# Optimization experiments

Hardware: AMD Instinct MI355X
Metric: run time of the kernel (lower is better)

## Reference

```python
import jax, jax.numpy as jnp
import numpy as np

N_HEAD = 16
N_EMBD = 2048
HEAD_DIM = N_EMBD // N_HEAD


def setup_inputs() -> dict:
    key = jax.random.key(0)
    kx, kqkv, kp = jax.random.split(key, 3)
    B, S = 2, 2048
    x = jax.random.normal(kx, (B, S, N_EMBD), dtype=jnp.float32)
    # torch nn.Linear weights, stored as [out, in]; y = x @ W.T
    scale = 1.0 / np.sqrt(N_EMBD)
    Wqkv = jax.random.uniform(kqkv, (3 * N_EMBD, N_EMBD), dtype=jnp.float32, minval=-scale, maxval=scale)
    Wproj = jax.random.uniform(kp, (N_EMBD, N_EMBD), dtype=jnp.float32, minval=-scale, maxval=scale)
    return {"x": x, "Wqkv": Wqkv, "Wproj": Wproj}


def reference(x, Wqkv, Wproj):
    B, S, E = x.shape
    qkv = x @ Wqkv.T  # [B,S,3E]
    q, k, v = jnp.split(qkv, 3, axis=2)
    # [B,H,S,D]
    q = q.reshape(B, S, N_HEAD, HEAD_DIM).transpose(0, 2, 1, 3)
    k = k.reshape(B, S, N_HEAD, HEAD_DIM).transpose(0, 2, 1, 3)
    v = v.reshape(B, S, N_HEAD, HEAD_DIM).transpose(0, 2, 1, 3)
    scores = jnp.einsum('bhqd,bhkd->bhqk', q, k) / jnp.sqrt(jnp.float32(HEAD_DIM))
    causal = jnp.tril(jnp.ones((S, S), dtype=bool))  # [S,S]
    scores = jnp.where(causal[None, None, :, :], scores, -jnp.inf)
    weights = jax.nn.softmax(scores, axis=-1)
    out = jnp.einsum('bhqk,bhkd->bhqd', weights, v)  # [B,H,S,D]
    out = out.transpose(0, 2, 1, 3).reshape(B, S, E)
    return out @ Wproj.T
```

## Files before the change

kernel.cpp:

```cpp
#include <hip/hip_runtime.h>
#include <cstdint>
#include <cstddef>

typedef __bf16 bf16;
typedef __bf16 bf16x8 __attribute__((ext_vector_type(8)));
typedef float  f32x4  __attribute__((ext_vector_type(4)));

static_assert(sizeof(bf16x8) == 16, "bf16x8 must be 16B");

__device__ __forceinline__ void async_copy16(const bf16* g, bf16* l) {
  __builtin_amdgcn_global_load_lds(
      (__attribute__((address_space(1))) void*)(g),
      (__attribute__((address_space(3))) void*)(l),
      16, 0, 0);
}

__device__ __forceinline__ uint32_t lds_u32(const bf16* p) {
  return (uint32_t)(uintptr_t)((__attribute__((address_space(3))) const bf16*)p);
}

__global__ __launch_bounds__(256)
void conv_f32_bf16(const float* __restrict__ s, bf16* __restrict__ d) {
  const size_t i = ((size_t)blockIdx.x * 256 + threadIdx.x) * 8;
  const f32x4 a = *(const f32x4*)(s + i);
  const f32x4 b = *(const f32x4*)(s + i + 4);
  bf16x8 o;
#pragma unroll
  for (int e = 0; e < 4; ++e) { o[e] = (bf16)a[e]; o[4 + e] = (bf16)b[e]; }
  *(bf16x8*)(d + i) = o;
}

template<int AMODE>
__device__ __forceinline__ void stageA32(const bf16* __restrict__ P, int K,
                                         int row0, int k0,
                                         bf16* lds, int wave, int lane) {
  const int lin0 = wave * 64;
  const int lin  = lin0 + lane;
  const int row  = lin >> 2;
  const int ch   = lin & 3;
  const int gch  = ch ^ ((row >> 1) & 3);
  const bf16* src;
  if constexpr (AMODE == 2) {
    const int rowA = row0 + row;
    const int b = rowA >> 11, s = rowA & 2047;
    src = P + ((size_t)(b * 16 + (k0 >> 7)) * 2048 + s) * 128 + (k0 & 127) + gch * 8;
  } else {
    src = P + (size_t)(row0 + row) * K + k0 + gch * 8;
  }
  async_copy16(src, lds + lin0 * 8);
}

__device__ __forceinline__ void stageW32(const bf16* __restrict__ P, int K,
                                         int row0, int k0,
                                         bf16* lds, int wave, int lane) {
#pragma unroll
  for (int i = 0; i < 2; ++i) {
    const int lin0 = i * 512 + wave * 64;
    const int lin  = lin0 + lane;
    const int row  = lin >> 2;
    const int ch   = lin & 3;
    const int gch  = ch ^ ((row >> 1) & 3);
    async_copy16(P + (size_t)(row0 + row) * K + k0 + gch * 8,
                 lds + lin0 * 8);
  }
}

__device__ __forceinline__ void ld_frags(uint32_t ab, uint32_t bb,
                                         bf16x8 (&a)[4], bf16x8 (&b)[4]) {
  asm volatile("ds_read_b128 %0, %1 offset:0"    : "=v"(a[0]) : "v"(ab));
  asm volatile("ds_read_b128 %0, %1 offset:1024" : "=v"(a[1]) : "v"(ab));
  asm volatile("ds_read_b128 %0, %1 offset:2048" : "=v"(a[2]) : "v"(ab));
  asm volatile("ds_read_b128 %0, %1 offset:3072" : "=v"(a[3]) : "v"(ab));
  asm volatile("ds_read_b128 %0, %1 offset:0"    : "=v"(b[0]) : "v"(bb));
  asm volatile("ds_read_b128 %0, %1 offset:1024" : "=v"(b[1]) : "v"(bb));
  asm volatile("ds_read_b128 %0, %1 offset:2048" : "=v"(b[2]) : "v"(bb));
  asm volatile("ds_read_b128 %0, %1 offset:3072" : "=v"(b[3]) : "v"(bb));
}

template<int AMODE, int CMODE>
__global__ __launch_bounds__(512, 2)
void gemm_bt3(const bf16* __restrict__ A, const bf16* __restrict__ W,
              float* __restrict__ Crow, bf16* __restrict__ Cq,
              bf16* __restrict__ Ck, bf16* __restrict__ Cvt,
              int M, int N, int K, int nbase) {
  __shared__ bf16 As[5][128 * 32];
  __shared__ bf16 Ws[5][256 * 32];

  const int tid  = threadIdx.x;
  const int wave = tid >> 6, lane = tid & 63;
  const int quad = lane >> 4, r = lane & 15;
  const int wr = wave >> 2, wc = wave & 3;

  const int gx  = gridDim.x;
  const int nwg = gx * gridDim.y;
  int wg = blockIdx.y * gx + blockIdx.x;
  wg = (wg & 7) * (nwg >> 3) + (wg >> 3);
  const int m0 = (wg / gx) * 128;
  const int n0 = (wg % gx) * 256;

  const int wm = wr * 64, wn = wc * 64;
  const int nT = K >> 5;
  const int cs = quad ^ ((r >> 1) & 3);

  f32x4 acc[4][4] = {};

  const uint32_t a_rd = lds_u32(&As[0][0]) + (((wm + r) * 32 + cs * 8) << 1);
  const uint32_t b_rd = lds_u32(&Ws[0][0]) + (((wn + r) * 32 + cs * 8) << 1);

#pragma unroll
  for (int i = 0; i < 4; ++i)
    if (i < nT) {
      stageA32<AMODE>(A, K, m0, i << 5, &As[i][0], wave, lane);
      stageW32(W, K, n0, i << 5, &Ws[i][0], wave, lane);
    }
  if (nT > 3)       asm volatile("s_waitcnt vmcnt(9)" ::: "memory");
  else if (nT == 3) asm volatile("s_waitcnt vmcnt(6)" ::: "memory");
  else if (nT == 2) asm volatile("s_waitcnt vmcnt(3)" ::: "memory");
  else              asm volatile("s_waitcnt vmcnt(0)" ::: "memory");
  __builtin_amdgcn_sched_barrier(0);
  __builtin_amdgcn_s_barrier();

  int bc = 0;
  int bs = 4;
  for (int t = 0; t < nT; ++t) {
    bf16x8 af[4], bw[4];
    ld_frags(a_rd + bc * 8192, b_rd + bc * 16384, af, bw);
    if (t + 4 < nT) {
      stageA32<AMODE>(A, K, m0, (t + 4) << 5, &As[bs][0], wave, lane);
      stageW32(W, K, n0, (t + 4) << 5, &Ws[bs][0], wave, lane);
      asm volatile("s_waitcnt vmcnt(9)" ::: "memory");
    } else if (t + 4 == nT) {
      asm volatile("s_waitcnt vmcnt(6)" ::: "memory");
    } else if (t + 3 == nT) {
      asm volatile("s_waitcnt vmcnt(3)" ::: "memory");
    } else {
      asm volatile("s_waitcnt vmcnt(0)" ::: "memory");
    }
    __builtin_amdgcn_sched_barrier(0);
    asm volatile("s_waitcnt lgkmcnt(0)" ::: "memory");
    __builtin_amdgcn_sched_barrier(0);
    __builtin_amdgcn_s_setprio(1);
#pragma unroll
    for (int m = 0; m < 4; ++m)
#pragma unroll
      for (int n = 0; n < 4; ++n)
        acc[m][n] = __builtin_amdgcn_mfma_f32_16x16x32_bf16(af[m], bw[n], acc[m][n], 0, 0, 0);
    __builtin_amdgcn_s_setprio(0);
    __builtin_amdgcn_s_barrier();
    bc = (bc + 1 == 5) ? 0 : bc + 1;
    bs = (bs + 1 == 5) ? 0 : bs + 1;
  }

#pragma unroll
  for (int i = 0; i < 4; ++i) {
    const int growb = m0 + wm + i * 16 + quad * 4;
#pragma unroll
    for (int j = 0; j < 4; ++j) {
      const int gcol = n0 + wn + j * 16 + r;
#pragma unroll
      for (int rg = 0; rg < 4; ++rg) {
        const int grow = growb + rg;
        if constexpr (CMODE == 1) {
          const int gc = nbase + gcol;
          const int which = gc >> 11;
          const int h = (gc >> 7) & 15;
          const int d = gc & 127;
          const int b = grow >> 11;
          const int s = grow & 2047;
          const bf16 v = (bf16)acc[i][j][rg];
          if (which == 0)
            Cq[(((size_t)b * 16 + h) * 2048 + s) * 128 + d] = v;
          else if (which == 1)
            Ck[(((size_t)b * 16 + h) * 2048 + s) * 128 + d] = v;
          else
            Cvt[(((size_t)b * 16 + h) * 128 + d) * 2048 + s] = v;
        } else {
          Crow[(size_t)grow * N + gcol] = acc[i][j][rg];
        }
      }
    }
  }
}

__global__ __launch_bounds__(256, 2)
void attn_kernel(bf16* __restrict__ Q, const bf16* __restrict__ K,
                 const bf16* __restrict__ Vt, int S) {
  __shared__ bf16 k_lds[2][64 * 128];
  __shared__ bf16 v_lds[2][128 * 64];
  __shared__ bf16 p_lds[4][16 * 64];

  const int tid = threadIdx.x, wave = tid >> 6, lane = tid & 63;
  const int quad = lane >> 4, r = lane & 15;
  const int bh = blockIdx.y;
  bf16* Qh = Q + (size_t)bh * S * 128;
  const bf16* Kh = K + (size_t)bh * S * 128;
  const bf16* Vth = Vt + (size_t)bh * 128 * S;

  const float sc = 0.0883883476483184f * 1.4426950408889634f;

  auto issue_stage = [&](int kv0, int buf) {
#pragma unroll
    for (int j = 0; j < 4; ++j) {
      const int lin0 = j * 256 + wave * 64;
      const int lin = lin0 + lane;
      const int row = lin >> 4, ch = lin & 15;
      async_copy16(Kh + (size_t)(kv0 + row) * 128 + ((ch ^ (row & 7)) << 3),
                   &k_lds[buf][0] + lin0 * 8);
    }
#pragma unroll
    for (int j = 0; j < 4; ++j) {
      const int lin0 = j * 256 + wave * 64;
      const int lin = lin0 + lane;
      const int row = lin >> 3, c = lin & 7;
      async_copy16(Vth + (size_t)row * S + kv0 + ((c ^ (row & 7)) << 3),
                   &v_lds[buf][0] + lin0 * 8);
    }
  };

  for (int pass = 0; pass < 2; ++pass) {
    const int qb = pass ? blockIdx.x : (31 - blockIdx.x);
    const int q0 = qb << 6;
    const int qrow0 = q0 + wave * 16;
    const int nkv = qb + 1;

    bf16x8 qf[4];
    for (int ks = 0; ks < 4; ++ks)
      qf[ks] = *(const bf16x8*)(Qh + (size_t)(qrow0 + r) * 128 + ks * 32 + quad * 8);

    f32x4 o_acc[8] = {};
    f32x4 m_run, l_run;
    for (int t = 0; t < 4; ++t) { m_run[t] = -1e30f; l_run[t] = 0.f; }

    issue_stage(0, 0);

    for (int kt = 0; kt < nkv; ++kt) {
      const int kv0 = kt << 6;
      const int cur = kt & 1;
      if (kt + 1 < nkv) {
        issue_stage((kt + 1) << 6, cur ^ 1);
        asm volatile("s_waitcnt vmcnt(8)" ::: "memory");
      } else {
        asm volatile("s_waitcnt vmcnt(0)" ::: "memory");
      }
      __builtin_amdgcn_sched_barrier(0);
      __syncthreads();

      {
        f32x4 sa[4] = {};
        __builtin_amdgcn_s_setprio(1);
        for (int ks = 0; ks < 4; ++ks) {
          bf16x8 kf[4];
          for (int nt = 0; nt < 4; ++nt) {
            const int kr = nt * 16 + r;
            kf[nt] = *(const bf16x8*)(&k_lds[cur][0] + kr * 128 + (((ks * 4 + quad) ^ (kr & 7)) << 3));
          }
          for (int nt = 0; nt < 4; ++nt)
            sa[nt] = __builtin_amdgcn_mfma_f32_16x16x32_bf16(qf[ks], kf[nt], sa[nt], 0, 0, 0);
        }
        __builtin_amdgcn_s_setprio(0);
        if (kv0 + 63 > qrow0) {
          for (int nt = 0; nt < 4; ++nt) {
            const int col  = kv0 + nt * 16 + r;
            const int rowb = qrow0 + quad * 4;
            for (int rg = 0; rg < 4; ++rg)
              if (col > rowb + rg) sa[nt][rg] = -1e30f;
          }
        }
        f32x4 mx = sa[0];
        for (int nt = 1; nt < 4; ++nt)
          for (int rg = 0; rg < 4; ++rg) mx[rg] = fmaxf(mx[rg], sa[nt][rg]);
        for (int off = 1; off < 16; off <<= 1)
          for (int rg = 0; rg < 4; ++rg) mx[rg] = fmaxf(mx[rg], __shfl_xor(mx[rg], off, 64));
        float need = mx[0] - m_run[0];
        for (int rg = 1; rg < 4; ++rg) need = fmaxf(need, mx[rg] - m_run[rg]);
        if (need * sc > 8.0f) {
          f32x4 alpha;
          for (int rg = 0; rg < 4; ++rg) {
            const float mnew = fmaxf(m_run[rg], mx[rg]);
            alpha[rg] = exp2f((m_run[rg] - mnew) * sc);
            m_run[rg] = mnew;
            l_run[rg] *= alpha[rg];
          }
          for (int nt2 = 0; nt2 < 8; ++nt2)
            for (int rg = 0; rg < 4; ++rg) o_acc[nt2][rg] *= alpha[rg];
        }
        f32x4 rsum = {0.f, 0.f, 0.f, 0.f};
        for (int nt = 0; nt < 4; ++nt)
          for (int rg = 0; rg < 4; ++rg) {
            const float p = exp2f((sa[nt][rg] - m_run[rg]) * sc);
            sa[nt][rg] = p;
            rsum[rg] += p;
          }
        for (int off = 1; off < 16; off <<= 1)
          for (int rg = 0; rg < 4; ++rg) rsum[rg] += __shfl_xor(rsum[rg], off, 64);
        for (int rg = 0; rg < 4; ++rg) l_run[rg] += rsum[rg];
        for (int nt = 0; nt < 4; ++nt)
          for (int rg = 0; rg < 4; ++rg) {
            const int prow = quad * 4 + rg;
            const int pcol = nt * 16 + r;
            p_lds[wave][prow * 64 + (((pcol >> 3) ^ (prow & 7)) * 8) + (pcol & 7)] =
                (bf16)sa[nt][rg];
          }
        __builtin_amdgcn_s_setprio(1);
        for (int ks2 = 0; ks2 < 2; ++ks2) {
          const int prow = r;
          const bf16x8 pf = *(const bf16x8*)(p_lds[wave] + prow * 64 + (((ks2 * 4 + quad) ^ (prow & 7)) * 8));
          for (int nt2 = 0; nt2 < 8; ++nt2) {
            const int vrow = nt2 * 16 + r;
            const bf16x8 vf = *(const bf16x8*)(&v_lds[cur][0] + vrow * 64 + (((ks2 * 4 + quad) ^ (vrow & 7)) * 8));
            o_acc[nt2] = __builtin_amdgcn_mfma_f32_16x16x32_bf16(pf, vf, o_acc[nt2], 0, 0, 0);
          }
        }
        __builtin_amdgcn_s_setprio(0);
      }
      __syncthreads();
    }

    f32x4 inv;
    for (int rg = 0; rg < 4; ++rg) inv[rg] = 1.0f / l_run[rg];
    for (int nt2 = 0; nt2 < 8; ++nt2) {
      const int d = nt2 * 16 + r;
      for (int rg = 0; rg < 4; ++rg) {
        const int s = qrow0 + quad * 4 + rg;
        Qh[(size_t)s * 128 + d] = (bf16)(o_acc[nt2][rg] * inv[rg]);
      }
    }
  }
}

extern "C" void kernel_launch(void* const* d_in, const int* in_sizes, int n_in,
                              void* d_out, int out_size, void* d_ws, size_t ws_size,
                              hipStream_t stream) {
  const float* x     = (const float*)d_in[0];
  const float* Wqkv  = (const float*)d_in[1];
  const float* Wproj = (const float*)d_in[2];
  float* out = (float*)d_out;

  const int Bm = 4096, E = 2048;
  const size_t plane = 8388608;

  bf16* qw  = (bf16*)d_ws;
  bf16* vtw = qw + plane;
  bf16* xb  = vtw + plane;
  bf16* kw  = (bf16*)d_out;
  bf16* wqb = kw + plane;

  conv_f32_bf16<<<8388608 / 2048, 256, 0, stream>>>(x, xb);
  for (int chunk = 0; chunk < 3; ++chunk) {
    conv_f32_bf16<<<4194304 / 2048, 256, 0, stream>>>(Wqkv + (size_t)chunk * 4194304, wqb);
    gemm_bt3<0, 1><<<dim3(2048 / 256, Bm / 128), 512, 0, stream>>>(
        xb, wqb, nullptr, qw, kw, vtw, Bm, 2048, E, chunk * 2048);
  }
  attn_kernel<<<dim3(16, 32), 256, 0, stream>>>(qw, kw, vtw, 2048);
  conv_f32_bf16<<<4194304 / 2048, 256, 0, stream>>>(Wproj, xb);
  gemm_bt3<2, 0><<<dim3(2048 / 256, Bm / 128), 512, 0, stream>>>(
      qw, xb, out, nullptr, nullptr, nullptr, Bm, 2048, E, 0);
}
```

Baseline: 401.0 us.

## Add 256x256 four-stage GEMM for output projection and split attention launch

Adds a new GEMM kernel with 256x256 tiles, a four-buffer async LDS pipeline, swizzled layout, workgroup remapping and explicit waitcnt scheduling. It replaces the 256x128 GEMM for the output projection. The attention launch is split into two launches of 8 query-block pairs each, using an added ibase offset. The larger tile increases operand reuse per byte loaded but uses more LDS, which limits occupancy, and the attention split adds a launch.

```diff
diff --git a/kernel.cpp b/kernel.cpp
--- a/kernel.cpp
+++ b/kernel.cpp
@@ -182,9 +182,150 @@
   }
 }
 
+template<int AMODE>
+__device__ __forceinline__ void stage256(const bf16* __restrict__ P, int K,
+                                         int row0, int k0,
+                                         bf16* lds, int wave, int lane) {
+#pragma unroll
+  for (int i = 0; i < 2; ++i) {
+    const int lin0 = i * 512 + wave * 64;
+    const int lin  = lin0 + lane;
+    const int row  = lin >> 2;
+    const int ch   = lin & 3;
+    const int gch  = ch ^ ((row >> 1) & 3);
+    const bf16* src;
+    if constexpr (AMODE == 2) {
+      const int rowA = row0 + row;
+      const int b = rowA >> 11, s = rowA & 2047;
+      src = P + ((size_t)(b * 16 + (k0 >> 7)) * 2048 + s) * 128 + (k0 & 127) + gch * 8;
+    } else {
+      src = P + (size_t)(row0 + row) * K + k0 + gch * 8;
+    }
+    async_copy16(src, lds + lin0 * 8);
+  }
+}
+
+__device__ __forceinline__ void ld_frags84(uint32_t ab, uint32_t bb,
+                                           bf16x8 (&a)[8], bf16x8 (&b)[4]) {
+  asm volatile("ds_read_b128 %0, %1 offset:0"    : "=v"(a[0]) : "v"(ab));
+  asm volatile("ds_read_b128 %0, %1 offset:1024" : "=v"(a[1]) : "v"(ab));
+  asm volatile("ds_read_b128 %0, %1 offset:2048" : "=v"(a[2]) : "v"(ab));
+  asm volatile("ds_read_b128 %0, %1 offset:3072" : "=v"(a[3]) : "v"(ab));
+  asm volatile("ds_read_b128 %0, %1 offset:4096" : "=v"(a[4]) : "v"(ab));
+  asm volatile("ds_read_b128 %0, %1 offset:5120" : "=v"(a[5]) : "v"(ab));
+  asm volatile("ds_read_b128 %0, %1 offset:6144" : "=v"(a[6]) : "v"(ab));
+  asm volatile("ds_read_b128 %0, %1 offset:7168" : "=v"(a[7]) : "v"(ab));
+  asm volatile("ds_read_b128 %0, %1 offset:0"    : "=v"(b[0]) : "v"(bb));
+  asm volatile("ds_read_b128 %0, %1 offset:1024" : "=v"(b[1]) : "v"(bb));
+  asm volatile("ds_read_b128 %0, %1 offset:2048" : "=v"(b[2]) : "v"(bb));
+  asm volatile("ds_read_b128 %0, %1 offset:3072" : "=v"(b[3]) : "v"(bb));
+}
+
+template<int AMODE, int CMODE>
+__global__ __launch_bounds__(512, 2)
+void gemm256r(const bf16* __restrict__ A, const bf16* __restrict__ W,
+              float* __restrict__ Crow, bf16* __restrict__ Cq,
+              bf16* __restrict__ Ck, bf16* __restrict__ Cvt,
+              int M, int N, int K, int nbase) {
+  __shared__ bf16 As[4][256 * 32];
+  __shared__ bf16 Ws[4][256 * 32];
+
+  const int tid  = threadIdx.x;
+  const int wave = tid >> 6, lane = tid & 63;
+  const int quad = lane >> 4, r = lane & 15;
+  const int wr = wave >> 2, wc = wave & 3;
+
+  const int gx  = gridDim.x;
+  const int nwg = gx * gridDim.y;
+  int wg = blockIdx.y * gx + blockIdx.x;
+  wg = (wg & 7) * (nwg >> 3) + (wg >> 3);
+  const int m0 = (wg / gx) * 256;
+  const int n0 = (wg % gx) * 256;
+
+  const int wm = wr * 128, wn = wc * 64;
+  const int nT = K >> 5;
+  const int cs = quad ^ ((r >> 1) & 3);
+
+  f32x4 acc[8][4] = {};
+
+  const uint32_t a_rd = lds_u32(&As[0][0]) + (((wm + r) * 32 + cs * 8) << 1);
+  const uint32_t b_rd = lds_u32(&Ws[0][0]) + (((wn + r) * 32 + cs * 8) << 1);
+
+#pragma unroll
+  for (int i = 0; i < 3; ++i)
+    if (i < nT) {
+      stage256<AMODE>(A, K, m0, i << 5, &As[i][0], wave, lane);
+      stage256<0>(W, K, n0, i << 5, &Ws[i][0], wave, lane);
+    }
+  if (nT > 2)       asm volatile("s_waitcnt vmcnt(8)" ::: "memory");
+  else if (nT == 2) asm volatile("s_waitcnt vmcnt(4)" ::: "memory");
+  else              asm volatile("s_waitcnt vmcnt(0)" ::: "memory");
+  __builtin_amdgcn_sched_barrier(0);
+  __builtin_amdgcn_s_barrier();
+
+  int bc = 0;
+  int bs = 3;
+  for (int t = 0; t < nT; ++t) {
+    bf16x8 af[8], bw[4];
+    ld_frags84(a_rd + bc * 16384, b_rd + bc * 16384, af, bw);
+    if (t + 3 < nT) {
+      stage256<AMODE>(A, K, m0, (t + 3) << 5, &As[bs][0], wave, lane);
+      stage256<0>(W, K, n0, (t + 3) << 5, &Ws[bs][0], wave, lane);
+      asm volatile("s_waitcnt vmcnt(8)" ::: "memory");
+    } else if (t + 3 == nT) {
+      asm volatile("s_waitcnt vmcnt(4)" ::: "memory");
+    } else {
+      asm volatile("s_waitcnt vmcnt(0)" ::: "memory");
+    }
+    __builtin_amdgcn_sched_barrier(0);
+    asm volatile("s_waitcnt lgkmcnt(0)" ::: "memory");
+    __builtin_amdgcn_sched_barrier(0);
+    __builtin_amdgcn_s_setprio(1);
+#pragma unroll
+    for (int m = 0; m < 8; ++m)
+#pragma unroll
+      for (int n = 0; n < 4; ++n)
+        acc[m][n] = __builtin_amdgcn_mfma_f32_16x16x32_bf16(af[m], bw[n], acc[m][n], 0, 0, 0);
+    __builtin_amdgcn_s_setprio(0);
+    __builtin_amdgcn_s_barrier();
+    bc = (bc + 1) & 3;
+    bs = (bs + 1) & 3;
+  }
+
+#pragma unroll
+  for (int i = 0; i < 8; ++i) {
+    const int growb = m0 + wm + i * 16 + quad * 4;
+#pragma unroll
+    for (int j = 0; j < 4; ++j) {
+      const int gcol = n0 + wn + j * 16 + r;
+#pragma unroll
+      for (int rg = 0; rg < 4; ++rg) {
+        const int grow = growb + rg;
+        if constexpr (CMODE == 1) {
+          const int gc = nbase + gcol;
+          const int which = gc >> 11;
+          const int h = (gc >> 7) & 15;
+          const int d = gc & 127;
+          const int b = grow >> 11;
+          const int s = grow & 2047;
+          const bf16 v = (bf16)acc[i][j][rg];
+          if (which == 0)
+            Cq[(((size_t)b * 16 + h) * 2048 + s) * 128 + d] = v;
+          else if (which == 1)
+            Ck[(((size_t)b * 16 + h) * 2048 + s) * 128 + d] = v;
+          else
+            Cvt[(((size_t)b * 16 + h) * 128 + d) * 2048 + s] = v;
+        } else {
+          Crow[(size_t)grow * N + gcol] = acc[i][j][rg];
+        }
+      }
+    }
+  }
+}
+
 __global__ __launch_bounds__(256, 2)
 void attn_kernel(bf16* __restrict__ Q, const bf16* __restrict__ K,
-                 const bf16* __restrict__ Vt, int S) {
+                 const bf16* __restrict__ Vt, int S, int ibase) {
   __shared__ bf16 k_lds[2][64 * 128];
   __shared__ bf16 v_lds[2][128 * 64];
   __shared__ bf16 p_lds[4][16 * 64];
@@ -217,8 +358,9 @@
     }
   };
 
+  const int i0 = ibase + blockIdx.x;
   for (int pass = 0; pass < 2; ++pass) {
-    const int qb = pass ? blockIdx.x : (31 - blockIdx.x);
+    const int qb = pass ? i0 : (31 - i0);
     const int q0 = qb << 6;
     const int qrow0 = q0 + wave * 16;
     const int nkv = qb + 1;
@@ -351,8 +493,9 @@
     gemm_bt3<0, 1><<<dim3(2048 / 256, Bm / 128), 512, 0, stream>>>(
         xb, wqb, nullptr, qw, kw, vtw, Bm, 2048, E, chunk * 2048);
   }
-  attn_kernel<<<dim3(16, 32), 256, 0, stream>>>(qw, kw, vtw, 2048);
+  attn_kernel<<<dim3(8, 32), 256, 0, stream>>>(qw, kw, vtw, 2048, 0);
+  attn_kernel<<<dim3(8, 32), 256, 0, stream>>>(qw, kw, vtw, 2048, 8);
   conv_f32_bf16<<<4194304 / 2048, 256, 0, stream>>>(Wproj, xb);
-  gemm_bt3<2, 0><<<dim3(2048 / 256, Bm / 128), 512, 0, stream>>>(
+  gemm256r<2, 0><<<dim3(2048 / 256, Bm / 256), 512, 0, stream>>>(
       qw, xb, out, nullptr, nullptr, nullptr, Bm, 2048, E, 0);
 }
```

Measured after the change: 478.1 us. 19.2% more time.

## Load K/V fragments directly from global memory and remap blocks for L2 locality

Applied to the files above, without the earlier changes.

Removes the double-buffered LDS staging of K and V tiles, with its async copies, waitcnts and block-wide barriers. Each wave now reads its MFMA operands straight from global memory, relying on L2/cache hits because the four waves share the same K/V rows. Block indices are also remapped so that blocks working on the same head are scheduled together. This trades away synchronization and LDS traffic for more global/L1 loads with exposed latency and no prefetch overlap.

```diff
diff --git a/kernel.cpp b/kernel.cpp
--- a/kernel.cpp
+++ b/kernel.cpp
@@ -185,40 +185,21 @@
 __global__ __launch_bounds__(256, 2)
 void attn_kernel(bf16* __restrict__ Q, const bf16* __restrict__ K,
                  const bf16* __restrict__ Vt, int S) {
-  __shared__ bf16 k_lds[2][64 * 128];
-  __shared__ bf16 v_lds[2][128 * 64];
   __shared__ bf16 p_lds[4][16 * 64];
 
   const int tid = threadIdx.x, wave = tid >> 6, lane = tid & 63;
   const int quad = lane >> 4, r = lane & 15;
-  const int bh = blockIdx.y;
+  const int bx = blockIdx.x, by = blockIdx.y;
+  const int bh = (bx & 7) * 4 + (by >> 3);
+  const int i0 = (by & 7) * 2 + (bx >> 3);
   bf16* Qh = Q + (size_t)bh * S * 128;
   const bf16* Kh = K + (size_t)bh * S * 128;
   const bf16* Vth = Vt + (size_t)bh * 128 * S;
 
   const float sc = 0.0883883476483184f * 1.4426950408889634f;
 
-  auto issue_stage = [&](int kv0, int buf) {
-#pragma unroll
-    for (int j = 0; j < 4; ++j) {
-      const int lin0 = j * 256 + wave * 64;
-      const int lin = lin0 + lane;
-      const int row = lin >> 4, ch = lin & 15;
-      async_copy16(Kh + (size_t)(kv0 + row) * 128 + ((ch ^ (row & 7)) << 3),
-                   &k_lds[buf][0] + lin0 * 8);
-    }
-#pragma unroll
-    for (int j = 0; j < 4; ++j) {
-      const int lin0 = j * 256 + wave * 64;
-      const int lin = lin0 + lane;
-      const int row = lin >> 3, c = lin & 7;
-      async_copy16(Vth + (size_t)row * S + kv0 + ((c ^ (row & 7)) << 3),
-                   &v_lds[buf][0] + lin0 * 8);
-    }
-  };
-
   for (int pass = 0; pass < 2; ++pass) {
-    const int qb = pass ? blockIdx.x : (31 - blockIdx.x);
+    const int qb = pass ? i0 : (31 - i0);
     const int q0 = qb << 6;
     const int qrow0 = q0 + wave * 16;
     const int nkv = qb + 1;
@@ -231,89 +212,80 @@
     f32x4 m_run, l_run;
     for (int t = 0; t < 4; ++t) { m_run[t] = -1e30f; l_run[t] = 0.f; }
 
-    issue_stage(0, 0);
-
     for (int kt = 0; kt < nkv; ++kt) {
       const int kv0 = kt << 6;
-      const int cur = kt & 1;
-      if (kt + 1 < nkv) {
-        issue_stage((kt + 1) << 6, cur ^ 1);
-        asm volatile("s_waitcnt vmcnt(8)" ::: "memory");
-      } else {
-        asm volatile("s_waitcnt vmcnt(0)" ::: "memory");
-      }
-      __builtin_amdgcn_sched_barrier(0);
-      __syncthreads();
-
-      {
-        f32x4 sa[4] = {};
-        __builtin_amdgcn_s_setprio(1);
-        for (int ks = 0; ks < 4; ++ks) {
-          bf16x8 kf[4];
-          for (int nt = 0; nt < 4; ++nt) {
-            const int kr = nt * 16 + r;
-            kf[nt] = *(const bf16x8*)(&k_lds[cur][0] + kr * 128 + (((ks * 4 + quad) ^ (kr & 7)) << 3));
-          }
-          for (int nt = 0; nt < 4; ++nt)
-            sa[nt] = __builtin_amdgcn_mfma_f32_16x16x32_bf16(qf[ks], kf[nt], sa[nt], 0, 0, 0);
-        }
-        __builtin_amdgcn_s_setprio(0);
-        if (kv0 + 63 > qrow0) {
-          for (int nt = 0; nt < 4; ++nt) {
-            const int col  = kv0 + nt * 16 + r;
-            const int rowb = qrow0 + quad * 4;
-            for (int rg = 0; rg < 4; ++rg)
-              if (col > rowb + rg) sa[nt][rg] = -1e30f;
-          }
-        }
-        f32x4 mx = sa[0];
-        for (int nt = 1; nt < 4; ++nt)
-          for (int rg = 0; rg < 4; ++rg) mx[rg] = fmaxf(mx[rg], sa[nt][rg]);
-        for (int off = 1; off < 16; off <<= 1)
-          for (int rg = 0; rg < 4; ++rg) mx[rg] = fmaxf(mx[rg], __shfl_xor(mx[rg], off, 64));
-        float need = mx[0] - m_run[0];
-        for (int rg = 1; rg < 4; ++rg) need = fmaxf(need, mx[rg] - m_run[rg]);
-        if (need * sc > 8.0f) {
-          f32x4 alpha;
-          for (int rg = 0; rg < 4; ++rg) {
-            const float mnew = fmaxf(m_run[rg], mx[rg]);
-            alpha[rg] = exp2f((m_run[rg] - mnew) * sc);
-            m_run[rg] = mnew;
-            l_run[rg] *= alpha[rg];
-          }
-          for (int nt2 = 0; nt2 < 8; ++nt2)
-            for (int rg = 0; rg < 4; ++rg) o_acc[nt2][rg] *= alpha[rg];
-        }
-        f32x4 rsum = {0.f, 0.f, 0.f, 0.f};
+
+      f32x4 sa[4] = {};
+      __builtin_amdgcn_s_setprio(1);
+      for (int ks = 0; ks < 4; ++ks) {
+        bf16x8 kf[4];
+#pragma unroll
         for (int nt = 0; nt < 4; ++nt)
-          for (int rg = 0; rg < 4; ++rg) {
-            const float p = exp2f((sa[nt][rg] - m_run[rg]) * sc);
-            sa[nt][rg] = p;
-            rsum[rg] += p;
-          }
-        for (int off = 1; off < 16; off <<= 1)
-          for (int rg = 0; rg < 4; ++rg) rsum[rg] += __shfl_xor(rsum[rg], off, 64);
-        for (int rg = 0; rg < 4; ++rg) l_run[rg] += rsum[rg];
+          kf[nt] = *(const bf16x8*)(Kh + (size_t)(kv0 + nt * 16 + r) * 128 + ks * 32 + quad * 8);
+#pragma unroll
         for (int nt = 0; nt < 4; ++nt)
-          for (int rg = 0; rg < 4; ++rg) {
-            const int prow = quad * 4 + rg;
-            const int pcol = nt * 16 + r;
-            p_lds[wave][prow * 64 + (((pcol >> 3) ^ (prow & 7)) * 8) + (pcol & 7)] =
-                (bf16)sa[nt][rg];
-          }
-        __builtin_amdgcn_s_setprio(1);
-        for (int ks2 = 0; ks2 < 2; ++ks2) {
-          const int prow = r;
-          const bf16x8 pf = *(const bf16x8*)(p_lds[wave] + prow * 64 + (((ks2 * 4 + quad) ^ (prow & 7)) * 8));
-          for (int nt2 = 0; nt2 < 8; ++nt2) {
-            const int vrow = nt2 * 16 + r;
-            const bf16x8 vf = *(const bf16x8*)(&v_lds[cur][0] + vrow * 64 + (((ks2 * 4 + quad) ^ (vrow & 7)) * 8));
-            o_acc[nt2] = __builtin_amdgcn_mfma_f32_16x16x32_bf16(pf, vf, o_acc[nt2], 0, 0, 0);
-          }
-        }
-        __builtin_amdgcn_s_setprio(0);
-      }
-      __syncthreads();
+          sa[nt] = __builtin_amdgcn_mfma_f32_16x16x32_bf16(qf[ks], kf[nt], sa[nt], 0, 0, 0);
+      }
+      __builtin_amdgcn_s_setprio(0);
+
+      if (kv0 + 63 > qrow0) {
+        for (int nt = 0; nt < 4; ++nt) {
+          const int col  = kv0 + nt * 16 + r;
+          const int rowb = qrow0 + quad * 4;
+          for (int rg = 0; rg < 4; ++rg)
+            if (col > rowb + rg) sa[nt][rg] = -1e30f;
+        }
+      }
+      f32x4 mx = sa[0];
+      for (int nt = 1; nt < 4; ++nt)
+        for (int rg = 0; rg < 4; ++rg) mx[rg] = fmaxf(mx[rg], sa[nt][rg]);
+      for (int off = 1; off < 16; off <<= 1)
+        for (int rg = 0; rg < 4; ++rg) mx[rg] = fmaxf(mx[rg], __shfl_xor(mx[rg], off, 64));
+      float need = mx[0] - m_run[0];
+      for (int rg = 1; rg < 4; ++rg) need = fmaxf(need, mx[rg] - m_run[rg]);
+      if (need * sc > 8.0f) {
+        f32x4 alpha;
+        for (int rg = 0; rg < 4; ++rg) {
+          const float mnew = fmaxf(m_run[rg], mx[rg]);
+          alpha[rg] = exp2f((m_run[rg] - mnew) * sc);
+          m_run[rg] = mnew;
+          l_run[rg] *= alpha[rg];
+        }
+        for (int nt2 = 0; nt2 < 8; ++nt2)
+          for (int rg = 0; rg < 4; ++rg) o_acc[nt2][rg] *= alpha[rg];
+      }
+      f32x4 rsum = {0.f, 0.f, 0.f, 0.f};
+      for (int nt = 0; nt < 4; ++nt)
+        for (int rg = 0; rg < 4; ++rg) {
+          const float p = exp2f((sa[nt][rg] - m_run[rg]) * sc);
+          sa[nt][rg] = p;
+          rsum[rg] += p;
+        }
+      for (int off = 1; off < 16; off <<= 1)
+        for (int rg = 0; rg < 4; ++rg) rsum[rg] += __shfl_xor(rsum[rg], off, 64);
+      for (int rg = 0; rg < 4; ++rg) l_run[rg] += rsum[rg];
+
+      for (int nt = 0; nt < 4; ++nt)
+        for (int rg = 0; rg < 4; ++rg) {
+          const int prow = quad * 4 + rg;
+          const int pcol = nt * 16 + r;
+          p_lds[wave][prow * 64 + (((pcol >> 3) ^ (prow & 7)) * 8) + (pcol & 7)] =
+              (bf16)sa[nt][rg];
+        }
+
+      __builtin_amdgcn_s_setprio(1);
+      for (int ks2 = 0; ks2 < 2; ++ks2) {
+        const int prow = r;
+        const bf16x8 pf = *(const bf16x8*)(p_lds[wave] + prow * 64 + (((ks2 * 4 + quad) ^ (prow & 7)) * 8));
+        bf16x8 vf[8];
+#pragma unroll
+        for (int nt2 = 0; nt2 < 8; ++nt2)
+          vf[nt2] = *(const bf16x8*)(Vth + (size_t)(nt2 * 16 + r) * S + kv0 + (ks2 * 4 + quad) * 8);
+#pragma unroll
+        for (int nt2 = 0; nt2 < 8; ++nt2)
+          o_acc[nt2] = __builtin_amdgcn_mfma_f32_16x16x32_bf16(pf, vf[nt2], o_acc[nt2], 0, 0, 0);
+      }
+      __builtin_amdgcn_s_setprio(0);
     }
 
     f32x4 inv;
```

New measurement: 572.3 us. +42.7%, slower.

## Single-buffer attention tiles, one q-tile per block, raise occupancy to four

Applied to the files above, without the earlier changes.

Attention blocks now each handle a single q tile, with the grid doubled and a swizzled q-tile assignment across heads for load balance. K/V LDS staging drops from double to single buffering, halving shared memory so launch bounds can request four blocks per CU. Waves whose rows lie entirely before the current KV tile skip the matmul work. The tradeoff is losing the prefetch overlap, so global load latency is now exposed and must be hidden by the extra resident blocks.

```diff
diff --git a/kernel.cpp b/kernel.cpp
--- a/kernel.cpp
+++ b/kernel.cpp
@@ -182,30 +182,37 @@
   }
 }
 
-__global__ __launch_bounds__(256, 2)
+__global__ __launch_bounds__(256, 4)
 void attn_kernel(bf16* __restrict__ Q, const bf16* __restrict__ K,
                  const bf16* __restrict__ Vt, int S) {
-  __shared__ bf16 k_lds[2][64 * 128];
-  __shared__ bf16 v_lds[2][128 * 64];
+  __shared__ bf16 k_lds[64 * 128];
+  __shared__ bf16 v_lds[128 * 64];
   __shared__ bf16 p_lds[4][16 * 64];
 
   const int tid = threadIdx.x, wave = tid >> 6, lane = tid & 63;
   const int quad = lane >> 4, r = lane & 15;
-  const int bh = blockIdx.y;
+  const int bx = blockIdx.x, by = blockIdx.y;
+  const int bh = by;
+  const int t4 = (by >> 3) & 3;
+  int qb;
+  if (t4 == 0)      qb = bx;
+  else if (t4 == 1) qb = 31 - bx;
+  else if (t4 == 2) qb = bx ^ 16;
+  else              qb = 31 - (bx ^ 16);
   bf16* Qh = Q + (size_t)bh * S * 128;
   const bf16* Kh = K + (size_t)bh * S * 128;
   const bf16* Vth = Vt + (size_t)bh * 128 * S;
 
   const float sc = 0.0883883476483184f * 1.4426950408889634f;
 
-  auto issue_stage = [&](int kv0, int buf) {
+  auto issue_stage = [&](int kv0) {
 #pragma unroll
     for (int j = 0; j < 4; ++j) {
       const int lin0 = j * 256 + wave * 64;
       const int lin = lin0 + lane;
       const int row = lin >> 4, ch = lin & 15;
       async_copy16(Kh + (size_t)(kv0 + row) * 128 + ((ch ^ (row & 7)) << 3),
-                   &k_lds[buf][0] + lin0 * 8);
+                   k_lds + lin0 * 8);
     }
 #pragma unroll
     for (int j = 0; j < 4; ++j) {
@@ -213,117 +220,107 @@
       const int lin = lin0 + lane;
       const int row = lin >> 3, c = lin & 7;
       async_copy16(Vth + (size_t)row * S + kv0 + ((c ^ (row & 7)) << 3),
-                   &v_lds[buf][0] + lin0 * 8);
+                   v_lds + lin0 * 8);
     }
   };
 
-  for (int pass = 0; pass < 2; ++pass) {
-    const int qb = pass ? blockIdx.x : (31 - blockIdx.x);
-    const int q0 = qb << 6;
-    const int qrow0 = q0 + wave * 16;
-    const int nkv = qb + 1;
-
-    bf16x8 qf[4];
-    for (int ks = 0; ks < 4; ++ks)
-      qf[ks] = *(const bf16x8*)(Qh + (size_t)(qrow0 + r) * 128 + ks * 32 + quad * 8);
-
-    f32x4 o_acc[8] = {};
-    f32x4 m_run, l_run;
-    for (int t = 0; t < 4; ++t) { m_run[t] = -1e30f; l_run[t] = 0.f; }
-
-    issue_stage(0, 0);
-
-    for (int kt = 0; kt < nkv; ++kt) {
-      const int kv0 = kt << 6;
-      const int cur = kt & 1;
-      if (kt + 1 < nkv) {
-        issue_stage((kt + 1) << 6, cur ^ 1);
-        asm volatile("s_waitcnt vmcnt(8)" ::: "memory");
-      } else {
-        asm volatile("s_waitcnt vmcnt(0)" ::: "memory");
-      }
-      __builtin_amdgcn_sched_barrier(0);
-      __syncthreads();
-
-      {
-        f32x4 sa[4] = {};
-        __builtin_amdgcn_s_setprio(1);
-        for (int ks = 0; ks < 4; ++ks) {
-          bf16x8 kf[4];
-          for (int nt = 0; nt < 4; ++nt) {
-            const int kr = nt * 16 + r;
-            kf[nt] = *(const bf16x8*)(&k_lds[cur][0] + kr * 128 + (((ks * 4 + quad) ^ (kr & 7)) << 3));
-          }
-          for (int nt = 0; nt < 4; ++nt)
-            sa[nt] = __builtin_amdgcn_mfma_f32_16x16x32_bf16(qf[ks], kf[nt], sa[nt], 0, 0, 0);
-        }
-        __builtin_amdgcn_s_setprio(0);
-        if (kv0 + 63 > qrow0) {
-          for (int nt = 0; nt < 4; ++nt) {
-            const int col  = kv0 + nt * 16 + r;
-            const int rowb = qrow0 + quad * 4;
-            for (int rg = 0; rg < 4; ++rg)
-              if (col > rowb + rg) sa[nt][rg] = -1e30f;
-          }
-        }
-        f32x4 mx = sa[0];
-        for (int nt = 1; nt < 4; ++nt)
-          for (int rg = 0; rg < 4; ++rg) mx[rg] = fmaxf(mx[rg], sa[nt][rg]);
-        for (int off = 1; off < 16; off <<= 1)
-          for (int rg = 0; rg < 4; ++rg) mx[rg] = fmaxf(mx[rg], __shfl_xor(mx[rg], off, 64));
-        float need = mx[0] - m_run[0];
-        for (int rg = 1; rg < 4; ++rg) need = fmaxf(need, mx[rg] - m_run[rg]);
-        if (need * sc > 8.0f) {
-          f32x4 alpha;
-          for (int rg = 0; rg < 4; ++rg) {
-            const float mnew = fmaxf(m_run[rg], mx[rg]);
-            alpha[rg] = exp2f((m_run[rg] - mnew) * sc);
-            m_run[rg] = mnew;
-            l_run[rg] *= alpha[rg];
-          }
-          for (int nt2 = 0; nt2 < 8; ++nt2)
-            for (int rg = 0; rg < 4; ++rg) o_acc[nt2][rg] *= alpha[rg];
-        }
-        f32x4 rsum = {0.f, 0.f, 0.f, 0.f};
+  const int q0 = qb << 6;
+  const int qrow0 = q0 + wave * 16;
+  const int nkv = qb + 1;
+
+  bf16x8 qf[4];
+  for (int ks = 0; ks < 4; ++ks)
+    qf[ks] = *(const bf16x8*)(Qh + (size_t)(qrow0 + r) * 128 + ks * 32 + quad * 8);
+
+  f32x4 o_acc[8] = {};
+  f32x4 m_run, l_run;
+  for (int t = 0; t < 4; ++t) { m_run[t] = -1e30f; l_run[t] = 0.f; }
+
+  for (int kt = 0; kt < nkv; ++kt) {
+    const int kv0 = kt << 6;
+    __syncthreads();
+    issue_stage(kv0);
+    asm volatile("s_waitcnt vmcnt(0)" ::: "memory");
+    __builtin_amdgcn_sched_barrier(0);
+    __syncthreads();
+
+    if (kv0 <= qrow0 + 15) {
+      f32x4 sa[4] = {};
+      __builtin_amdgcn_s_setprio(1);
+      for (int ks = 0; ks < 4; ++ks) {
+        bf16x8 kf[4];
+        for (int nt = 0; nt < 4; ++nt) {
+          const int kr = nt * 16 + r;
+          kf[nt] = *(const bf16x8*)(k_lds + kr * 128 + (((ks * 4 + quad) ^ (kr & 7)) << 3));
+        }
         for (int nt = 0; nt < 4; ++nt)
-          for (int rg = 0; rg < 4; ++rg) {
-            const float p = exp2f((sa[nt][rg] - m_run[rg]) * sc);
-            sa[nt][rg] = p;
-            rsum[rg] += p;
-          }
-        for (int off = 1; off < 16; off <<= 1)
-          for (int rg = 0; rg < 4; ++rg) rsum[rg] += __shfl_xor(rsum[rg], off, 64);
-        for (int rg = 0; rg < 4; ++rg) l_run[rg] += rsum[rg];
-        for (int nt = 0; nt < 4; ++nt)
-          for (int rg = 0; rg < 4; ++rg) {
-            const int prow = quad * 4 + rg;
-            const int pcol = nt * 16 + r;
-            p_lds[wave][prow * 64 + (((pcol >> 3) ^ (prow & 7)) * 8) + (pcol & 7)] =
-                (bf16)sa[nt][rg];
-          }
-        __builtin_amdgcn_s_setprio(1);
-        for (int ks2 = 0; ks2 < 2; ++ks2) {
-          const int prow = r;
-          const bf16x8 pf = *(const bf16x8*)(p_lds[wave] + prow * 64 + (((ks2 * 4 + quad) ^ (prow & 7)) * 8));
-          for (int nt2 = 0; nt2 < 8; ++nt2) {
-            const int vrow = nt2 * 16 + r;
-            const bf16x8 vf = *(const bf16x8*)(&v_lds[cur][0] + vrow * 64 + (((ks2 * 4 + quad) ^ (vrow & 7)) * 8));
-            o_acc[nt2] = __builtin_amdgcn_mfma_f32_16x16x32_bf16(pf, vf, o_acc[nt2], 0, 0, 0);
-          }
-        }
-        __builtin_amdgcn_s_setprio(0);
-      }
-      __syncthreads();
-    }
-
-    f32x4 inv;
-    for (int rg = 0; rg < 4; ++rg) inv[rg] = 1.0f / l_run[rg];
-    for (int nt2 = 0; nt2 < 8; ++nt2) {
-      const int d = nt2 * 16 + r;
-      for (int rg = 0; rg < 4; ++rg) {
-        const int s = qrow0 + quad * 4 + rg;
-        Qh[(size_t)s * 128 + d] = (bf16)(o_acc[nt2][rg] * inv[rg]);
-      }
+          sa[nt] = __builtin_amdgcn_mfma_f32_16x16x32_bf16(qf[ks], kf[nt], sa[nt], 0, 0, 0);
+      }
+      __builtin_amdgcn_s_setprio(0);
+      if (kv0 + 63 > qrow0) {
+        for (int nt = 0; nt < 4; ++nt) {
+          const int col  = kv0 + nt * 16 + r;
+          const int rowb = qrow0 + quad * 4;
+          for (int rg = 0; rg < 4; ++rg)
+            if (col > rowb + rg) sa[nt][rg] = -1e30f;
+        }
+      }
+      f32x4 mx = sa[0];
+      for (int nt = 1; nt < 4; ++nt)
+        for (int rg = 0; rg < 4; ++rg) mx[rg] = fmaxf(mx[rg], sa[nt][rg]);
+      for (int off = 1; off < 16; off <<= 1)
+        for (int rg = 0; rg < 4; ++rg) mx[rg] = fmaxf(mx[rg], __shfl_xor(mx[rg], off, 64));
+      float need = mx[0] - m_run[0];
+      for (int rg = 1; rg < 4; ++rg) need = fmaxf(need, mx[rg] - m_run[rg]);
+      if (need * sc > 8.0f) {
+        f32x4 alpha;
+        for (int rg = 0; rg < 4; ++rg) {
+          const float mnew = fmaxf(m_run[rg], mx[rg]);
+          alpha[rg] = exp2f((m_run[rg] - mnew) * sc);
+          m_run[rg] = mnew;
+          l_run[rg] *= alpha[rg];
+        }
+        for (int nt2 = 0; nt2 < 8; ++nt2)
+          for (int rg = 0; rg < 4; ++rg) o_acc[nt2][rg] *= alpha[rg];
+      }
+      f32x4 rsum = {0.f, 0.f, 0.f, 0.f};
+      for (int nt = 0; nt < 4; ++nt)
+        for (int rg = 0; rg < 4; ++rg) {
+          const float p = exp2f((sa[nt][rg] - m_run[rg]) * sc);
+          sa[nt][rg] = p;
+          rsum[rg] += p;
+        }
+      for (int off = 1; off < 16; off <<= 1)
+        for (int rg = 0; rg < 4; ++rg) rsum[rg] += __shfl_xor(rsum[rg], off, 64);
+      for (int rg = 0; rg < 4; ++rg) l_run[rg] += rsum[rg];
+      for (int nt = 0; nt < 4; ++nt)
+        for (int rg = 0; rg < 4; ++rg) {
+          const int prow = quad * 4 + rg;
+          const int pcol = nt * 16 + r;
+          p_lds[wave][prow * 64 + (((pcol >> 3) ^ (prow & 7)) * 8) + (pcol & 7)] =
+              (bf16)sa[nt][rg];
+        }
+      __builtin_amdgcn_s_setprio(1);
+      for (int ks2 = 0; ks2 < 2; ++ks2) {
+        const int prow = r;
+        const bf16x8 pf = *(const bf16x8*)(p_lds[wave] + prow * 64 + (((ks2 * 4 + quad) ^ (prow & 7)) * 8));
+        for (int nt2 = 0; nt2 < 8; ++nt2) {
+          const int vrow = nt2 * 16 + r;
+          const bf16x8 vf = *(const bf16x8*)(v_lds + vrow * 64 + (((ks2 * 4 + quad) ^ (vrow & 7)) * 8));
+          o_acc[nt2] = __builtin_amdgcn_mfma_f32_16x16x32_bf16(pf, vf, o_acc[nt2], 0, 0, 0);
+        }
+      }
+      __builtin_amdgcn_s_setprio(0);
+    }
+  }
+
+  f32x4 inv;
+  for (int rg = 0; rg < 4; ++rg) inv[rg] = 1.0f / l_run[rg];
+  for (int nt2 = 0; nt2 < 8; ++nt2) {
+    const int d = nt2 * 16 + r;
+    for (int rg = 0; rg < 4; ++rg) {
+      const int s = qrow0 + quad * 4 + rg;
+      Qh[(size_t)s * 128 + d] = (bf16)(o_acc[nt2][rg] * inv[rg]);
     }
   }
 }
@@ -351,7 +348,7 @@
     gemm_bt3<0, 1><<<dim3(2048 / 256, Bm / 128), 512, 0, stream>>>(
         xb, wqb, nullptr, qw, kw, vtw, Bm, 2048, E, chunk * 2048);
   }
-  attn_kernel<<<dim3(16, 32), 256, 0, stream>>>(qw, kw, vtw, 2048);
+  attn_kernel<<<dim3(32, 32), 256, 0, stream>>>(qw, kw, vtw, 2048);
   conv_f32_bf16<<<4194304 / 2048, 256, 0, stream>>>(Wproj, xb);
   gemm_bt3<2, 0><<<dim3(2048 / 256, Bm / 128), 512, 0, stream>>>(
       qw, xb, out, nullptr, nullptr, nullptr, Bm, 2048, E, 0);
```

Result: slower. 448.3 us (+11.8%).
